# Optimization experiments

Measured on AMD Instinct MI355X. Metric: run time of the kernel, lower is better.

The kernel has to match this reference:

```python
import jax, jax.numpy as jnp
import numpy as np

EMBED_DIM = 1024
HEAD_DIM = 64


def setup_inputs() -> dict:
    key = jax.random.key(0)
    ks = jax.random.split(key, 7)
    B, S = 4, 2048
    s = 1.0 / np.sqrt(EMBED_DIM)
    h = jax.random.normal(ks[0], (B, S, EMBED_DIM), dtype=jnp.float32)
    Wq = jax.random.normal(ks[1], (EMBED_DIM, HEAD_DIM), dtype=jnp.float32) * s
    bq = jax.random.normal(ks[2], (HEAD_DIM,), dtype=jnp.float32) * 0.01
    Wk = jax.random.normal(ks[3], (EMBED_DIM, HEAD_DIM), dtype=jnp.float32) * s
    bk = jax.random.normal(ks[4], (HEAD_DIM,), dtype=jnp.float32) * 0.01
    Wv = jax.random.normal(ks[5], (EMBED_DIM, HEAD_DIM), dtype=jnp.float32) * s
    bv = jax.random.normal(ks[6], (HEAD_DIM,), dtype=jnp.float32) * 0.01
    return {"h": h, "Wq": Wq, "bq": bq, "Wk": Wk, "bk": bk, "Wv": Wv, "bv": bv}


def reference(h, Wq, bq, Wk, bk, Wv, bv):
    # Linear projections: h [B,S,E] -> q,k [B,S,D]
    q = jnp.einsum("bse,ed->bsd", h, Wq) + bq
    k = jnp.einsum("bse,ed->bsd", h, Wk) + bk
    v = jnp.einsum("bse,ed->bsd", h, Wv) + bv  # computed but UNUSED (faithful to source)
    del v
    scale = 1.0 / jnp.sqrt(jnp.asarray(HEAD_DIM, dtype=q.dtype))
    # scores [B, Sq, Sk]
    scores = jnp.einsum("bqd,bkd->bqk", q, k) * scale
    # NOTE: source uses softmax over dim=1 (query axis), not the key axis
    weights = jax.nn.softmax(scores, axis=1)
    # NOTE: source passes h (not v) as the value tensor
    out = jnp.einsum("bqk,bke->bqe", weights, h)  # [B, Sq, E]
    return out
```

## Files before the change

### kernel.cpp

```cpp
#include <hip/hip_runtime.h>
#include <hip/hip_bf16.h>
#include <math.h>

#define EMBED 1024
#define HDIM  64
#define BATCH 4
#define SEQ   2048

typedef __attribute__((ext_vector_type(8))) short short8;
typedef __attribute__((ext_vector_type(4))) float f32x4;
typedef unsigned int u32;
typedef unsigned short u16;

static __device__ __forceinline__ u16 f2bf(float f) {
    union { float f; u32 u; } v; v.f = f;
    u32 r = v.u + 0x7fffu + ((v.u >> 16) & 1u);
    return (u16)(r >> 16);
}

static __device__ __forceinline__ void gload_lds16(const u16* g, u16* l) {
    __builtin_amdgcn_global_load_lds(
        (const __attribute__((address_space(1))) u32*)g,
        (__attribute__((address_space(3))) u32*)l, 16, 0, 0);
}

__global__ __launch_bounds__(256) void wt_kernel(
    const float* __restrict__ Wq, const float* __restrict__ Wk,
    u16* __restrict__ WqT, u16* __restrict__ WkT)
{
    __shared__ float tile[64][65];
    const float* W = blockIdx.y ? Wk : Wq;
    u16* WT = blockIdx.y ? WkT : WqT;
    int e0 = blockIdx.x * 64;
    int t = threadIdx.x, c = t & 63, r4 = t >> 6;
    for (int r = r4; r < 64; r += 4)
        tile[r][c] = W[(size_t)(e0 + r) * HDIM + c];
    __syncthreads();
    for (int d = r4; d < 64; d += 4)
        WT[(size_t)d * EMBED + e0 + c] = f2bf(tile[c][d]);
}

__global__ __launch_bounds__(256) void proj_kernel(
    const float* __restrict__ h, const u16* __restrict__ WqT, const u16* __restrict__ WkT,
    const float* __restrict__ bq, const float* __restrict__ bk,
    u16* __restrict__ Qbf, u16* __restrict__ Kbf)
{
    __shared__ u16 hs[2][16][136];
    int b = blockIdx.x >> 7, s0 = (blockIdx.x & 127) * 16;
    int t = threadIdx.x, lane = t & 63, w = t >> 6;
    int l15 = lane & 15, quad = lane >> 4;
    int pj = w >> 1, nh = (w & 1) * 32;
    const float* hb = h + ((size_t)b * SEQ + s0) * EMBED;
    const u16* Wp = pj ? WkT : WqT;
    int r = t >> 4, c4 = (t & 15) * 4;

    f32x4 preA0 = *(const f32x4*)(hb + (size_t)r * EMBED + c4);
    f32x4 preA1 = *(const f32x4*)(hb + (size_t)r * EMBED + 64 + c4);
    f32x4 preB0 = *(const f32x4*)(hb + (size_t)r * EMBED + 128 + c4);
    f32x4 preB1 = *(const f32x4*)(hb + (size_t)r * EMBED + 192 + c4);
    f32x4 accA[2], accB[2];
    accA[0] = accA[1] = accB[0] = accB[1] = (f32x4){0.f, 0.f, 0.f, 0.f};

    const u16* Wrow0 = Wp + (size_t)(nh + l15) * EMBED;
    const u16* Wrow1 = Wp + (size_t)(nh + 16 + l15) * EMBED;

    short8 cw[8];
#pragma unroll
    for (int i = 0; i < 4; i++) {
        cw[i]     = *(const short8*)(Wrow0 + i * 32 + quad * 8);
        cw[4 + i] = *(const short8*)(Wrow1 + i * 32 + quad * 8);
    }

    for (int it = 0; it < 8; ++it) {
        int ec = it * 128, buf = it & 1;
        uint2 pk;
        pk.x = (u32)f2bf(preA0[0]) | ((u32)f2bf(preA0[1]) << 16);
        pk.y = (u32)f2bf(preA0[2]) | ((u32)f2bf(preA0[3]) << 16);
        *(uint2*)&hs[buf][r][c4] = pk;
        pk.x = (u32)f2bf(preA1[0]) | ((u32)f2bf(preA1[1]) << 16);
        pk.y = (u32)f2bf(preA1[2]) | ((u32)f2bf(preA1[3]) << 16);
        *(uint2*)&hs[buf][r][64 + c4] = pk;
        __syncthreads();

        preA0 = preB0; preA1 = preB1;
        if (it + 2 < 8) {
            preB0 = *(const f32x4*)(hb + (size_t)r * EMBED + ec + 256 + c4);
            preB1 = *(const f32x4*)(hb + (size_t)r * EMBED + ec + 320 + c4);
        }
        short8 nw[8];
#pragma unroll
        for (int i = 0; i < 8; i++) nw[i] = cw[i];
        if (it + 1 < 8) {
#pragma unroll
            for (int i = 0; i < 4; i++) {
                nw[i]     = *(const short8*)(Wrow0 + ec + 128 + i * 32 + quad * 8);
                nw[4 + i] = *(const short8*)(Wrow1 + ec + 128 + i * 32 + quad * 8);
            }
        }

        short8 a0 = *(const short8*)&hs[buf][l15][quad * 8];
        short8 a1 = *(const short8*)&hs[buf][l15][32 + quad * 8];
        short8 a2 = *(const short8*)&hs[buf][l15][64 + quad * 8];
        short8 a3 = *(const short8*)&hs[buf][l15][96 + quad * 8];
        accA[0] = __builtin_amdgcn_mfma_f32_16x16x32_bf16(a0, cw[0], accA[0], 0, 0, 0);
        accA[1] = __builtin_amdgcn_mfma_f32_16x16x32_bf16(a0, cw[4], accA[1], 0, 0, 0);
        accB[0] = __builtin_amdgcn_mfma_f32_16x16x32_bf16(a1, cw[1], accB[0], 0, 0, 0);
        accB[1] = __builtin_amdgcn_mfma_f32_16x16x32_bf16(a1, cw[5], accB[1], 0, 0, 0);
        accA[0] = __builtin_amdgcn_mfma_f32_16x16x32_bf16(a2, cw[2], accA[0], 0, 0, 0);
        accA[1] = __builtin_amdgcn_mfma_f32_16x16x32_bf16(a2, cw[6], accA[1], 0, 0, 0);
        accB[0] = __builtin_amdgcn_mfma_f32_16x16x32_bf16(a3, cw[3], accB[0], 0, 0, 0);
        accB[1] = __builtin_amdgcn_mfma_f32_16x16x32_bf16(a3, cw[7], accB[1], 0, 0, 0);
#pragma unroll
        for (int i = 0; i < 8; i++) cw[i] = nw[i];
    }

    const float* bias = pj ? bk : bq;
    float scale = pj ? 1.0f : 0.125f;
    u16* outp = pj ? Kbf : Qbf;
    float bv0 = bias[nh + l15], bv1 = bias[nh + 16 + l15];
#pragma unroll
    for (int rr = 0; rr < 4; rr++) {
        size_t row = (size_t)b * SEQ + s0 + quad * 4 + rr;
        outp[row * HDIM + nh + l15]      = f2bf((accA[0][rr] + accB[0][rr] + bv0) * scale);
        outp[row * HDIM + nh + 16 + l15] = f2bf((accA[1][rr] + accB[1][rr] + bv1) * scale);
    }
}

__global__ __launch_bounds__(256) void sw_kernel(
    const u16* __restrict__ Qbf, const u16* __restrict__ Kbf,
    u16* __restrict__ Wmat, float* __restrict__ invl)
{
    __shared__ float sl[4][16];
    int b = blockIdx.y;
    int k0 = blockIdx.x * 16;
    int t = threadIdx.x, lane = t & 63, w = t >> 6;
    int l15 = lane & 15, quad = lane >> 4;
    const u16* Qb = Qbf + (size_t)b * SEQ * HDIM;
    const u16* Kb = Kbf + (size_t)b * SEQ * HDIM;
    u16* Wb = Wmat + (size_t)b * SEQ * SEQ;
    short8 kf0 = *(const short8*)(Kb + (size_t)(k0 + l15) * HDIM + quad * 8);
    short8 kf1 = *(const short8*)(Kb + (size_t)(k0 + l15) * HDIM + 32 + quad * 8);
    f32x4 lacc = {0.f, 0.f, 0.f, 0.f};
    int qs = w * 512;
    const u16* qpa = Qb + (size_t)(qs + l15) * HDIM;
    const u16* qpb = Qb + (size_t)(qs + 16 + l15) * HDIM;
    short8 cf0a = *(const short8*)(qpa + quad * 8);
    short8 cf1a = *(const short8*)(qpa + 32 + quad * 8);
    short8 cf0b = *(const short8*)(qpb + quad * 8);
    short8 cf1b = *(const short8*)(qpb + 32 + quad * 8);

    for (int q0 = qs; q0 < qs + 512; q0 += 32) {
        short8 nf0a = cf0a, nf1a = cf1a, nf0b = cf0b, nf1b = cf1b;
        if (q0 + 32 < qs + 512) {
            const u16* na = Qb + (size_t)(q0 + 32 + l15) * HDIM;
            const u16* nb = Qb + (size_t)(q0 + 48 + l15) * HDIM;
            nf0a = *(const short8*)(na + quad * 8);
            nf1a = *(const short8*)(na + 32 + quad * 8);
            nf0b = *(const short8*)(nb + quad * 8);
            nf1b = *(const short8*)(nb + 32 + quad * 8);
        }
        f32x4 aa = {0.f, 0.f, 0.f, 0.f}, ab = {0.f, 0.f, 0.f, 0.f};
        aa = __builtin_amdgcn_mfma_f32_16x16x32_bf16(kf0, cf0a, aa, 0, 0, 0);
        ab = __builtin_amdgcn_mfma_f32_16x16x32_bf16(kf0, cf0b, ab, 0, 0, 0);
        aa = __builtin_amdgcn_mfma_f32_16x16x32_bf16(kf1, cf1a, aa, 0, 0, 0);
        ab = __builtin_amdgcn_mfma_f32_16x16x32_bf16(kf1, cf1b, ab, 0, 0, 0);
        float e0 = __expf(aa[0]), e1 = __expf(aa[1]);
        float e2 = __expf(aa[2]), e3 = __expf(aa[3]);
        float g0 = __expf(ab[0]), g1 = __expf(ab[1]);
        float g2 = __expf(ab[2]), g3 = __expf(ab[3]);
        lacc[0] += e0 + g0; lacc[1] += e1 + g1;
        lacc[2] += e2 + g2; lacc[3] += e3 + g3;
        uint2 pa, pb;
        pa.x = (u32)f2bf(e0) | ((u32)f2bf(e1) << 16);
        pa.y = (u32)f2bf(e2) | ((u32)f2bf(e3) << 16);
        pb.x = (u32)f2bf(g0) | ((u32)f2bf(g1) << 16);
        pb.y = (u32)f2bf(g2) | ((u32)f2bf(g3) << 16);
        *(uint2*)(Wb + (size_t)(q0 + l15) * SEQ + k0 + quad * 4) = pa;
        *(uint2*)(Wb + (size_t)(q0 + 16 + l15) * SEQ + k0 + quad * 4) = pb;
        cf0a = nf0a; cf1a = nf1a; cf0b = nf0b; cf1b = nf1b;
    }
#pragma unroll
    for (int m = 1; m <= 8; m <<= 1) {
        lacc[0] += __shfl_xor(lacc[0], m, 64);
        lacc[1] += __shfl_xor(lacc[1], m, 64);
        lacc[2] += __shfl_xor(lacc[2], m, 64);
        lacc[3] += __shfl_xor(lacc[3], m, 64);
    }
    if (l15 == 0) {
        sl[w][quad * 4 + 0] = lacc[0];
        sl[w][quad * 4 + 1] = lacc[1];
        sl[w][quad * 4 + 2] = lacc[2];
        sl[w][quad * 4 + 3] = lacc[3];
    }
    __syncthreads();
    if (t < 16)
        invl[b * SEQ + k0 + t] =
            1.0f / ((sl[0][t] + sl[1][t]) + (sl[2][t] + sl[3][t]));
}

__global__ __launch_bounds__(256) void tscale_kernel(
    const float* __restrict__ h, const float* __restrict__ invl,
    u16* __restrict__ hT)
{
    __shared__ float tile[64][65];
    int b  = blockIdx.z;
    int s0 = blockIdx.x * 64, e0 = blockIdx.y * 64;
    int t = threadIdx.x;
    int r16 = t >> 4, c4 = (t & 15) * 4;
    const float* hb = h + (size_t)b * SEQ * EMBED;
#pragma unroll
    for (int rr = r16; rr < 64; rr += 16) {
        f32x4 v = *(const f32x4*)(hb + (size_t)(s0 + rr) * EMBED + e0 + c4);
        *(f32x4*)&tile[rr][c4] = v;
    }
    __syncthreads();
    f32x4 il4 = *(const f32x4*)(invl + b * SEQ + s0 + c4);
    u16* hTb = hT + (size_t)b * EMBED * SEQ;
#pragma unroll
    for (int er = r16; er < 64; er += 16) {
        u16 p0 = f2bf(tile[c4 + 0][er] * il4[0]);
        u16 p1 = f2bf(tile[c4 + 1][er] * il4[1]);
        u16 p2 = f2bf(tile[c4 + 2][er] * il4[2]);
        u16 p3 = f2bf(tile[c4 + 3][er] * il4[3]);
        uint2 pk;
        pk.x = (u32)p0 | ((u32)p1 << 16);
        pk.y = (u32)p2 | ((u32)p3 << 16);
        *(uint2*)(hTb + (size_t)(e0 + er) * SEQ + s0 + c4) = pk;
    }
}

__global__ __launch_bounds__(512, 2) void out_gemm_kernel(
    const u16* __restrict__ Wmat, const u16* __restrict__ hT, float* __restrict__ out)
{
    __shared__ __align__(16) char smem[3 * 49152];
#define ASLOT(si) ((u16*)(smem + (size_t)(si) * 49152))
#define BSLOT(si) ((u16*)(smem + (size_t)(si) * 49152 + 32768))
    int b = blockIdx.z;
    int q0 = blockIdx.x * 256, e0 = blockIdx.y * 128;
    int t = threadIdx.x, lane = t & 63, w = t >> 6;
    int l15 = lane & 15, quad = lane >> 4;
    const u16* Wb  = Wmat + (size_t)b * SEQ * SEQ;
    const u16* hTb = hT + (size_t)b * EMBED * SEQ;
    int kf = w >> 2;
    int wm = (w >> 1) & 1, wn = w & 1;
    int wq = wm * 128, we = wn * 64;

    f32x4 acc[8][4];
#pragma unroll
    for (int i = 0; i < 8; i++)
#pragma unroll
        for (int j = 0; j < 4; j++) acc[i][j] = (f32x4){0.f, 0.f, 0.f, 0.f};

    int st_rl = lane >> 3;
    int st_pc = lane & 7;

#define STAGE_A(si, k0, ld)                                                    \
    {                                                                          \
        int rowb = w * 32 + (ld) * 8;                                          \
        int row  = rowb + st_rl;                                               \
        int cg   = st_pc ^ (row & 7);                \
        gload_lds16(Wb + (size_t)(q0 + row) * SEQ + (k0) + cg * 8,             \
                    ASLOT(si) + rowb * 64 + lane * 8);                         \
    }
#define STAGE_B(si, k0, ld)                                                    \
    {                                                                          \
        int rowb = w * 16 + (ld) * 8;                                          \
        int row  = rowb + st_rl;                                               \
        int cg   = st_pc ^ (row & 7);                                          \
        gload_lds16(hTb + (size_t)(e0 + row) * SEQ + (k0) + cg * 8,            \
                    BSLOT(si) + rowb * 64 + lane * 8);                         \
    }

#define LDFRAGS_A(i0)                                                          \
    {                                                                          \
        _Pragma("unroll")                                                      \
        for (int ii = 0; ii < 4; ii++) {                                       \
            int ra  = wq + ((i0) + ii) * 16 + l15;                             \
            int pca = (kf * 4 + quad) ^ (ra & 7);                              \
            af[ii] = *(const short8*)(Ab + ra * 64 + pca * 8);                 \
        }                                                                      \
    }
#define LDFRAGS_B                                                              \
    {                                                                          \
        _Pragma("unroll")                                                      \
        for (int j = 0; j < 4; j++) {                                          \
            int rb  = we + j * 16 + l15;                                       \
            int pcb = (kf * 4 + quad) ^ (rb & 7);                              \
            bfr[j] = *(const short8*)(Bb + rb * 64 + pcb * 8);                 \
        }                                                                      \
    }

#define MFMA16(i0)                                                             \
    {                                                                          \
        _Pragma("unroll")                                                      \
        for (int ii = 0; ii < 4; ii++)                                         \
            _Pragma("unroll")                                                  \
            for (int j = 0; j < 4; j++)                                        \
                acc[(i0) + ii][j] = __builtin_amdgcn_mfma_f32_16x16x32_bf16(   \
                    af[ii], bfr[j], acc[(i0) + ii][j], 0, 0, 0);               \
    }

    STAGE_A(0, 0, 0) STAGE_A(0, 0, 1) STAGE_A(0, 0, 2) STAGE_A(0, 0, 3)
    STAGE_B(0, 0, 0) STAGE_B(0, 0, 1)
    STAGE_A(1, 64, 0) STAGE_A(1, 64, 1) STAGE_A(1, 64, 2) STAGE_A(1, 64, 3)
    STAGE_B(1, 64, 0) STAGE_B(1, 64, 1)
    asm volatile("s_waitcnt vmcnt(6)" ::: "memory");
    __builtin_amdgcn_s_barrier();

    for (int kt = 0; kt < 32; ++kt) {
        int s = kt % 3;
        const u16* Ab = ASLOT(s);
        const u16* Bb = BSLOT(s);
        int s2 = (kt + 2) % 3;
        int k2 = (kt + 2) * 64 + kf * 0;
        bool st = (kt + 2) < 32;
        short8 af[4], bfr[4];

        LDFRAGS_A(0)
        LDFRAGS_B
        if (st) { STAGE_A(s2, k2, 0) STAGE_A(s2, k2, 1) STAGE_B(s2, k2, 0) }
        __builtin_amdgcn_s_barrier();
        asm volatile("s_waitcnt lgkmcnt(0)" ::: "memory");
        __builtin_amdgcn_sched_barrier(0);
        __builtin_amdgcn_s_setprio(1);
        MFMA16(0)
        __builtin_amdgcn_s_setprio(0);
        __builtin_amdgcn_s_barrier();

        LDFRAGS_A(4)
        if (st) { STAGE_A(s2, k2, 2) STAGE_A(s2, k2, 3) STAGE_B(s2, k2, 1) }
        __builtin_amdgcn_s_barrier();
        asm volatile("s_waitcnt lgkmcnt(0)" ::: "memory");
        __builtin_amdgcn_sched_barrier(0);
        __builtin_amdgcn_s_setprio(1);
        MFMA16(4)
        __builtin_amdgcn_s_setprio(0);
        if (kt < 30)       { asm volatile("s_waitcnt vmcnt(6)" ::: "memory"); }
        else if (kt == 30) { asm volatile("s_waitcnt vmcnt(0)" ::: "memory"); }
        __builtin_amdgcn_s_barrier();
    }
#undef STAGE_A
#undef STAGE_B
#undef LDFRAGS_A
#undef LDFRAGS_B
#undef MFMA16

    float* red = (float*)smem;
    if (w >= 4) {
        float* reg = red + (size_t)(w & 3) * 8192;
#pragma unroll
        for (int i = 0; i < 8; i++)
#pragma unroll
            for (int j = 0; j < 4; j++)
                *(f32x4*)(reg + ((i * 4 + j) * 64 + lane) * 4) = acc[i][j];
    }
    __syncthreads();
    if (w < 4) {
        float* reg = red + (size_t)w * 8192;
        float* outb = out + (size_t)b * SEQ * EMBED;
#pragma unroll
        for (int i = 0; i < 8; i++)
#pragma unroll
            for (int j = 0; j < 4; j++) {
                f32x4 o = *(const f32x4*)(reg + ((i * 4 + j) * 64 + lane) * 4);
                o += acc[i][j];
#pragma unroll
                for (int r = 0; r < 4; r++)
                    outb[(size_t)(q0 + wq + i * 16 + quad * 4 + r) * EMBED
                         + e0 + we + j * 16 + l15] = o[r];
            }
    }
#undef ASLOT
#undef BSLOT
}

extern "C" void kernel_launch(void* const* d_in, const int* in_sizes, int n_in,
                              void* d_out, int out_size, void* d_ws, size_t ws_size,
                              hipStream_t stream) {
    (void)in_sizes; (void)n_in; (void)out_size; (void)ws_size;
    const float* h  = (const float*)d_in[0];
    const float* Wq = (const float*)d_in[1];
    const float* bq = (const float*)d_in[2];
    const float* Wk = (const float*)d_in[3];
    const float* bk = (const float*)d_in[4];
    float* out = (float*)d_out;

    char* ws = (char*)d_ws;
    u16*   Qbf  = (u16*)(ws);
    u16*   Kbf  = (u16*)(ws + (1ull << 20));
    u16*   hT   = (u16*)(ws + (2ull << 20));
    float* invl = (float*)(ws + (18ull << 20));
    u16*   WqT  = (u16*)(ws + (18ull << 20) + (128ull << 10));
    u16*   WkT  = (u16*)(ws + (18ull << 20) + (256ull << 10));
    u16*   Wmat = (u16*)(ws + (19ull << 20));

    hipLaunchKernelGGL(wt_kernel, dim3(16, 2), dim3(256), 0, stream, Wq, Wk, WqT, WkT);
    hipLaunchKernelGGL(proj_kernel, dim3(512), dim3(256), 0, stream,
                       h, WqT, WkT, bq, bk, Qbf, Kbf);
    hipLaunchKernelGGL(sw_kernel, dim3(128, 4), dim3(256), 0, stream,
                       Qbf, Kbf, Wmat, invl);
    hipLaunchKernelGGL(tscale_kernel, dim3(32, 16, 4), dim3(256), 0, stream,
                       h, invl, hT);
    hipLaunchKernelGGL(out_gemm_kernel, dim3(8, 8, 4), dim3(512), 0, stream,
                       Wmat, hT, out);
}
```

Before: 174.0 us.

## Unroll out-GEMM K loop by three, precompute addresses and drop mid-tile barriers

Unrolls the 32-step K loop of the output GEMM into groups of three so the triple-buffer slot indices become compile-time constants. Global and LDS addresses are computed once and advanced by pointer increments instead of being recomputed each step. The two mid-iteration barriers, the explicit lgkmcnt waits and the sched_barrier are removed, keeping one barrier per tile. This cuts address arithmetic and synchronisation stalls, but leaves LDS-wait placement and instruction scheduling to the compiler, which may interleave the MFMAs less well.

```diff
diff --git a/kernel.cpp b/kernel.cpp
--- a/kernel.cpp
+++ b/kernel.cpp
@@ -233,8 +233,6 @@
     const u16* __restrict__ Wmat, const u16* __restrict__ hT, float* __restrict__ out)
 {
     __shared__ __align__(16) char smem[3 * 49152];
-#define ASLOT(si) ((u16*)(smem + (size_t)(si) * 49152))
-#define BSLOT(si) ((u16*)(smem + (size_t)(si) * 49152 + 32768))
     int b = blockIdx.z;
     int q0 = blockIdx.x * 256, e0 = blockIdx.y * 128;
     int t = threadIdx.x, lane = t & 63, w = t >> 6;
@@ -254,40 +252,55 @@
     int st_rl = lane >> 3;
     int st_pc = lane & 7;
 
-#define STAGE_A(si, k0, ld)                                                    \
+    const u16* gA[4];
+    const u16* gB[2];
+#pragma unroll
+    for (int ld = 0; ld < 4; ld++) {
+        int row = w * 32 + ld * 8 + st_rl;
+        int cg  = st_pc ^ (row & 7);
+        gA[ld] = Wb + (size_t)(q0 + row) * SEQ + cg * 8;
+    }
+#pragma unroll
+    for (int ld = 0; ld < 2; ld++) {
+        int row = w * 16 + ld * 8 + st_rl;
+        int cg  = st_pc ^ (row & 7);
+        gB[ld] = hTb + (size_t)(e0 + row) * SEQ + cg * 8;
+    }
+    int dA[4], dB[2];
+#pragma unroll
+    for (int ld = 0; ld < 4; ld++) dA[ld] = (w * 32 + ld * 8) * 128 + lane * 16;
+#pragma unroll
+    for (int ld = 0; ld < 2; ld++) dB[ld] = 32768 + (w * 16 + ld * 8) * 128 + lane * 16;
+    int offA[8], offB[4];
+#pragma unroll
+    for (int ii = 0; ii < 8; ii++) {
+        int ra  = wq + ii * 16 + l15;
+        int pca = (kf * 4 + quad) ^ (ra & 7);
+        offA[ii] = ra * 128 + pca * 16;
+    }
+#pragma unroll
+    for (int j = 0; j < 4; j++) {
+        int rb  = we + j * 16 + l15;
+        int pcb = (kf * 4 + quad) ^ (rb & 7);
+        offB[j] = 32768 + rb * 128 + pcb * 16;
+    }
+
+#define STAGE_H1(si)                                                           \
     {                                                                          \
-        int rowb = w * 32 + (ld) * 8;                                          \
-        int row  = rowb + st_rl;                                               \
-        int cg   = st_pc ^ (row & 7);                \
-        gload_lds16(Wb + (size_t)(q0 + row) * SEQ + (k0) + cg * 8,             \
-                    ASLOT(si) + rowb * 64 + lane * 8);                         \
-    }
-#define STAGE_B(si, k0, ld)                                                    \
+        gload_lds16(gA[0], (u16*)(smem + (si) * 49152 + dA[0]));               \
+        gload_lds16(gA[1], (u16*)(smem + (si) * 49152 + dA[1]));               \
+        gload_lds16(gB[0], (u16*)(smem + (si) * 49152 + dB[0]));               \
+    }
+#define STAGE_H2(si)                                                           \
     {                                                                          \
-        int rowb = w * 16 + (ld) * 8;                                          \
-        int row  = rowb + st_rl;                                               \
-        int cg   = st_pc ^ (row & 7);                                          \
-        gload_lds16(hTb + (size_t)(e0 + row) * SEQ + (k0) + cg * 8,            \
-                    BSLOT(si) + rowb * 64 + lane * 8);                         \
-    }
-
-#define LDFRAGS_A(i0)                                                          \
+        gload_lds16(gA[2], (u16*)(smem + (si) * 49152 + dA[2]));               \
+        gload_lds16(gA[3], (u16*)(smem + (si) * 49152 + dA[3]));               \
+        gload_lds16(gB[1], (u16*)(smem + (si) * 49152 + dB[1]));               \
+    }
+#define ADV()                                                                  \
     {                                                                          \
-        _Pragma("unroll")                                                      \
-        for (int ii = 0; ii < 4; ii++) {                                       \
-            int ra  = wq + ((i0) + ii) * 16 + l15;                             \
-            int pca = (kf * 4 + quad) ^ (ra & 7);                              \
-            af[ii] = *(const short8*)(Ab + ra * 64 + pca * 8);                 \
-        }                                                                      \
-    }
-#define LDFRAGS_B                                                              \
-    {                                                                          \
-        _Pragma("unroll")                                                      \
-        for (int j = 0; j < 4; j++) {                                          \
-            int rb  = we + j * 16 + l15;                                       \
-            int pcb = (kf * 4 + quad) ^ (rb & 7);                              \
-            bfr[j] = *(const short8*)(Bb + rb * 64 + pcb * 8);                 \
-        }                                                                      \
+        gA[0] += 64; gA[1] += 64; gA[2] += 64; gA[3] += 64;                    \
+        gB[0] += 64; gB[1] += 64;                                              \
     }
 
 #define MFMA16(i0)                                                             \
@@ -300,49 +313,48 @@
                     af[ii], bfr[j], acc[(i0) + ii][j], 0, 0, 0);               \
     }
 
-    STAGE_A(0, 0, 0) STAGE_A(0, 0, 1) STAGE_A(0, 0, 2) STAGE_A(0, 0, 3)
-    STAGE_B(0, 0, 0) STAGE_B(0, 0, 1)
-    STAGE_A(1, 64, 0) STAGE_A(1, 64, 1) STAGE_A(1, 64, 2) STAGE_A(1, 64, 3)
-    STAGE_B(1, 64, 0) STAGE_B(1, 64, 1)
+#define TILE(si, si2, DO_STAGE, VMC)                                           \
+    {                                                                          \
+        const char* Sb = smem + (si) * 49152;                                  \
+        short8 af[4], bfr[4];                                                  \
+        _Pragma("unroll")                                                      \
+        for (int ii = 0; ii < 4; ii++)                                         \
+            af[ii] = *(const short8*)(Sb + offA[ii]);                          \
+        _Pragma("unroll")                                                      \
+        for (int j = 0; j < 4; j++)                                            \
+            bfr[j] = *(const short8*)(Sb + offB[j]);                           \
+        if (DO_STAGE) STAGE_H1(si2)                                            \
+        __builtin_amdgcn_s_setprio(1);                                         \
+        MFMA16(0)                                                              \
+        __builtin_amdgcn_s_setprio(0);                                         \
+        _Pragma("unroll")                                                      \
+        for (int ii = 0; ii < 4; ii++)                                         \
+            af[ii] = *(const short8*)(Sb + offA[4 + ii]);                      \
+        if (DO_STAGE) { STAGE_H2(si2) ADV() }                                  \
+        __builtin_amdgcn_s_setprio(1);                                         \
+        MFMA16(4)                                                              \
+        __builtin_amdgcn_s_setprio(0);                                         \
+        if ((VMC) == 6) { asm volatile("s_waitcnt vmcnt(6)" ::: "memory"); }   \
+        else if ((VMC) == 0) { asm volatile("s_waitcnt vmcnt(0)" ::: "memory"); } \
+        __builtin_amdgcn_s_barrier();                                          \
+    }
+
+    STAGE_H1(0) STAGE_H2(0) ADV()
+    STAGE_H1(1) STAGE_H2(1) ADV()
     asm volatile("s_waitcnt vmcnt(6)" ::: "memory");
     __builtin_amdgcn_s_barrier();
 
-    for (int kt = 0; kt < 32; ++kt) {
-        int s = kt % 3;
-        const u16* Ab = ASLOT(s);
-        const u16* Bb = BSLOT(s);
-        int s2 = (kt + 2) % 3;
-        int k2 = (kt + 2) * 64 + kf * 0;
-        bool st = (kt + 2) < 32;
-        short8 af[4], bfr[4];
-
-        LDFRAGS_A(0)
-        LDFRAGS_B
-        if (st) { STAGE_A(s2, k2, 0) STAGE_A(s2, k2, 1) STAGE_B(s2, k2, 0) }
-        __builtin_amdgcn_s_barrier();
-        asm volatile("s_waitcnt lgkmcnt(0)" ::: "memory");
-        __builtin_amdgcn_sched_barrier(0);
-        __builtin_amdgcn_s_setprio(1);
-        MFMA16(0)
-        __builtin_amdgcn_s_setprio(0);
-        __builtin_amdgcn_s_barrier();
-
-        LDFRAGS_A(4)
-        if (st) { STAGE_A(s2, k2, 2) STAGE_A(s2, k2, 3) STAGE_B(s2, k2, 1) }
-        __builtin_amdgcn_s_barrier();
-        asm volatile("s_waitcnt lgkmcnt(0)" ::: "memory");
-        __builtin_amdgcn_sched_barrier(0);
-        __builtin_amdgcn_s_setprio(1);
-        MFMA16(4)
-        __builtin_amdgcn_s_setprio(0);
-        if (kt < 30)       { asm volatile("s_waitcnt vmcnt(6)" ::: "memory"); }
-        else if (kt == 30) { asm volatile("s_waitcnt vmcnt(0)" ::: "memory"); }
-        __builtin_amdgcn_s_barrier();
-    }
-#undef STAGE_A
-#undef STAGE_B
-#undef LDFRAGS_A
-#undef LDFRAGS_B
+    for (int g = 0; g < 10; ++g) {
+        TILE(0, 2, true, 6)
+        TILE(1, 0, true, 6)
+        TILE(2, 1, true, 6)
+    }
+    TILE(0, 2, false, 0)
+    TILE(1, 0, false, -1)
+#undef TILE
+#undef STAGE_H1
+#undef STAGE_H2
+#undef ADV
 #undef MFMA16
 
     float* red = (float*)smem;
@@ -370,8 +382,6 @@
                          + e0 + we + j * 16 + l15] = o[r];
             }
     }
-#undef ASLOT
-#undef BSLOT
 }
 
 extern "C" void kernel_launch(void* const* d_in, const int* in_sizes, int n_in,
```

Result: no change. 173.9 us (-0.1%).
